# Performance work log

Hardware: AMD Instinct MI355X
Metric: run time of the kernel (lower is better)

The kernel has to match this reference:

```python
import jax, jax.numpy as jnp
import numpy as np

S = 2   # upsample scale
K = 5   # reassembly kernel k_up


def setup_inputs() -> dict:
    key = jax.random.key(0)
    ks = jax.random.split(key, 7)
    B, C, H, W = 4, 128, 64, 64
    C_MID = 64
    return {
        "x": jax.random.normal(ks[0], (B, C, H, W), dtype=jnp.float32),
        "w1": jax.random.normal(ks[1], (C_MID, C), dtype=jnp.float32) * 0.05,
        "w2": jax.random.normal(ks[2], (S * S * K * K, C_MID, 3, 3), dtype=jnp.float32) * 0.05,
        "bn_gamma": jax.random.uniform(ks[3], (C_MID,), dtype=jnp.float32, minval=0.5, maxval=1.5),
        "bn_beta": jax.random.normal(ks[4], (C_MID,), dtype=jnp.float32) * 0.1,
        "bn_mean": jax.random.normal(ks[5], (C_MID,), dtype=jnp.float32) * 0.1,
        "bn_var": jax.random.uniform(ks[6], (C_MID,), dtype=jnp.float32, minval=0.5, maxval=1.5),
    }


def reference(x, w1, w2, bn_gamma, bn_beta, bn_mean, bn_var):
    B, C, H, W = x.shape
    s, k = S, K
    eps = 1e-5
    # --- content encoder: 1x1 conv -> BN (inference form) -> ReLU -> 3x3 conv ---
    h = jnp.einsum('bchw,oc->bohw', x, w1)  # (B, c_mid, H, W)
    inv = bn_gamma / jnp.sqrt(bn_var + eps)
    h = h * inv[None, :, None, None] + (bn_beta - bn_mean * inv)[None, :, None, None]
    h = jax.nn.relu(h)
    ker = jax.lax.conv_general_dilated(
        h, w2, window_strides=(1, 1), padding=((1, 1), (1, 1)),
        dimension_numbers=('NCHW', 'OIHW', 'NCHW'))  # (B, s*s*k*k, H, W)
    # softmax over the k*k reassembly window
    ker = jax.nn.softmax(ker.reshape(B, s * s, k * k, H, W), axis=2)
    # --- unfold k x k neighborhoods of x (row-major window order, as F.unfold) ---
    p = k // 2
    xp = jnp.pad(x, ((0, 0), (0, 0), (p, p), (p, p)))
    patches = jnp.stack(
        [xp[:, :, i:i + H, j:j + W] for i in range(k) for j in range(k)],
        axis=2)  # (B, C, k*k, H, W)
    # weighted reassembly: sum over the k*k window per (sub-pixel, channel)
    out = jnp.einsum('bckhw,bskhw->bcshw', patches, ker)  # (B, C, s*s, H, W)
    # pixel shuffle: (B, C, s, s, H, W) -> (B, C, H*s, W*s)
    out = out.reshape(B, C, s, s, H, W).transpose(0, 1, 4, 2, 5, 3)
    return out.reshape(B, C, H * s, W * s)
```

## Files before the change

kernel.cpp:

```cpp
#include <hip/hip_runtime.h>
#include <hip/hip_bf16.h>

#define HW 4096

typedef __attribute__((ext_vector_type(8))) short  short8;
typedef __attribute__((ext_vector_type(4))) float  floatx4;

#define OFF_W2B 0ul
#define OFF_W1B 129024ul
#define OFF_BN  145408ul

__global__ __launch_bounds__(256) void prep_kernel(const float* __restrict__ w1,
                                                   const float* __restrict__ w2,
                                                   const float* __restrict__ gamma,
                                                   const float* __restrict__ beta,
                                                   const float* __restrict__ mean,
                                                   const float* __restrict__ var,
                                                   char* __restrict__ ws) {
    int tid = blockIdx.x * 256 + threadIdx.x;
    if (tid < 64512) {
        int n = tid / 576;
        int k = tid - n * 576;
        int t = k >> 6, c = k & 63;
        float v = (n < 100) ? w2[(n * 64 + c) * 9 + t] : 0.f;
        ((__hip_bfloat16*)(ws + OFF_W2B))[tid] = __float2bfloat16(v);
    } else if (tid < 64512 + 8192) {
        int i = tid - 64512;
        ((__hip_bfloat16*)(ws + OFF_W1B))[i] = __float2bfloat16(w1[i]);
    } else if (tid < 64512 + 8192 + 64) {
        int o = tid - 64512 - 8192;
        float inv = gamma[o] * rsqrtf(var[o] + 1e-5f);
        ((float2*)(ws + OFF_BN))[o] = make_float2(inv, beta[o] - mean[o] * inv);
    }
}

__global__ __launch_bounds__(1024, 1) void fused_carafe(const float* __restrict__ x,
                                                        const char* __restrict__ ws,
                                                        float* __restrict__ out) {
    __shared__ float xs[128 * 144];
    __shared__ __align__(16) __hip_bfloat16 hs[100 * 88];
    __shared__ __align__(16) char un[54784];
    __hip_bfloat16* xbh = (__hip_bfloat16*)un;
    float* lg = (float*)un;
    float* ks = (float*)(un + 29184);

    int b    = blockIdx.x >> 6;
    int tile = blockIdx.x & 63;
    int ty0 = (tile >> 3) << 3;
    int tx0 = (tile & 7) << 3;
    int tid = threadIdx.x;
    int lane = tid & 63, wave = tid >> 6;
    int q = lane >> 4, m = lane & 15;

    int nh  = wave & 1;
    int nt0 = nh * 2;
    const __hip_bfloat16* w1b = (const __hip_bfloat16*)(ws + OFF_W1B);
    short8 bw[2][4];
    #pragma unroll
    for (int j = 0; j < 2; ++j)
        #pragma unroll
        for (int s = 0; s < 4; ++s)
            bw[j][s] = *(const short8*)(w1b + ((nt0 + j) * 16 + m) * 128 + s * 32 + q * 8);

    const float* xb = x + (size_t)b * 128 * HW;
    #pragma unroll
    for (int i = 0; i < 18; ++i) {
        int idx = tid + i * 1024;
        int c = idx / 144, p = idx - c * 144;
        int hy = p / 12, hx = p - hy * 12;
        int gy = ty0 + hy - 2, gx = tx0 + hx - 2;
        float v = 0.f;
        if ((unsigned)gy < 64u && (unsigned)gx < 64u)
            v = xb[(size_t)c * HW + gy * 64 + gx];
        xs[idx] = v;
        if ((unsigned)(hy - 1) < 10u && (unsigned)(hx - 1) < 10u) {
            int hp = (hy - 1) * 10 + (hx - 1);
            xbh[hp * 136 + c] = __float2bfloat16(v);
        }
    }
    if (tid < 816) ((unsigned*)(xbh + 100 * 136))[tid] = 0u;
    __syncthreads();

    if (wave < 14) {
        int mt = wave >> 1;
        int pix = mt * 16 + m;
        floatx4 acc0, acc1;
        #pragma unroll
        for (int r = 0; r < 4; ++r) { acc0[r] = 0.f; acc1[r] = 0.f; }
        #pragma unroll
        for (int s = 0; s < 4; ++s) {
            short8 a = *(const short8*)(&xbh[pix * 136 + s * 32 + q * 8]);
            acc0 = __builtin_amdgcn_mfma_f32_16x16x32_bf16(a, bw[0][s], acc0, 0, 0, 0);
            acc1 = __builtin_amdgcn_mfma_f32_16x16x32_bf16(a, bw[1][s], acc1, 0, 0, 0);
        }
        const float2* bn = (const float2*)(ws + OFF_BN);
        int o0 = nt0 * 16 + m, o1 = (nt0 + 1) * 16 + m;
        float2 ia0 = bn[o0], ia1 = bn[o1];
        #pragma unroll
        for (int r = 0; r < 4; ++r) {
            int prow = mt * 16 + q * 4 + r;
            if (prow < 100) {
                int hy = prow / 10, hx = prow - hy * 10;
                int gy = ty0 + hy - 1, gx = tx0 + hx - 1;
                bool in = ((unsigned)gy < 64u) && ((unsigned)gx < 64u);
                float v0 = in ? fmaxf(fmaf(acc0[r], ia0.x, ia0.y), 0.f) : 0.f;
                float v1 = in ? fmaxf(fmaf(acc1[r], ia1.x, ia1.y), 0.f) : 0.f;
                hs[prow * 88 + o0] = __float2bfloat16(v0);
                hs[prow * 88 + o1] = __float2bfloat16(v1);
            }
        }
    }
    __syncthreads();

    {
        int mt = wave & 3, ng = wave >> 2;
        int pixidx = mt * 16 + m;
        int py = pixidx >> 3, px = pixidx & 7;
        int cn0 = ng * 2;
        int NT = (ng < 3) ? 2 : 1;

        const __hip_bfloat16* w2b = (const __hip_bfloat16*)(ws + OFF_W2B);
        const __hip_bfloat16* bp0 = w2b + (size_t)(cn0 * 16 + m) * 576 + q * 8;
        const __hip_bfloat16* bp1 = w2b + (size_t)((cn0 + 1) * 16 + m) * 576 + q * 8;

        floatx4 acc0, acc1;
        #pragma unroll
        for (int r = 0; r < 4; ++r) { acc0[r] = 0.f; acc1[r] = 0.f; }

        short8 b0 = *(const short8*)bp0;
        short8 b1 = (NT == 2) ? *(const short8*)bp1 : b0;

        for (int s = 0; s < 18; ++s) {
            int t = s >> 1, c0 = (s & 1) * 32;
            short8 a = *(const short8*)(&hs[((py + t / 3) * 10 + (px + t % 3)) * 88 + c0 + q * 8]);
            short8 n0 = b0, n1 = b1;
            if (s < 17) {
                int ko = (s + 1) * 32;
                n0 = *(const short8*)(bp0 + ko);
                if (NT == 2) n1 = *(const short8*)(bp1 + ko);
            }
            acc0 = __builtin_amdgcn_mfma_f32_16x16x32_bf16(a, b0, acc0, 0, 0, 0);
            if (NT == 2)
                acc1 = __builtin_amdgcn_mfma_f32_16x16x32_bf16(a, b1, acc1, 0, 0, 0);
            b0 = n0; b1 = n1;
        }
        #pragma unroll
        for (int r = 0; r < 4; ++r)
            lg[(mt * 16 + q * 4 + r) * 114 + cn0 * 16 + m] = acc0[r];
        if (NT == 2) {
            #pragma unroll
            for (int r = 0; r < 4; ++r)
                lg[(mt * 16 + q * 4 + r) * 114 + (cn0 + 1) * 16 + m] = acc1[r];
        }
    }
    __syncthreads();

    if (tid < 256) {
        int pix = tid & 63, g = tid >> 6;
        float v[25];
        #pragma unroll
        for (int wi = 0; wi < 25; ++wi) v[wi] = lg[pix * 114 + g * 25 + wi];
        float mx = v[0];
        #pragma unroll
        for (int wi = 1; wi < 25; ++wi) mx = fmaxf(mx, v[wi]);
        float ssum = 0.f;
        #pragma unroll
        for (int wi = 0; wi < 25; ++wi) { v[wi] = __expf(v[wi] - mx); ssum += v[wi]; }
        float rs = 1.f / ssum;
        #pragma unroll
        for (int t25 = 0; t25 < 25; ++t25)
            ks[(t25 * 4 + g) * 64 + pix] = v[t25] * rs;
    }
    __syncthreads();

    {
        int ch0 = wave * 8;
        int py = lane >> 3, px = lane & 7;
        int Y = ty0 + py, X = tx0 + px;

        float acc[32];
        #pragma unroll
        for (int i = 0; i < 32; ++i) acc[i] = 0.f;

        const float* xw = xs + ch0 * 144 + py * 12 + px;
        #pragma unroll 5
        for (int t = 0; t < 25; ++t) {
            int ti = t / 5, tj = t % 5;
            int po = ti * 12 + tj;
            float k0 = ks[(t * 4 + 0) * 64 + lane];
            float k1 = ks[(t * 4 + 1) * 64 + lane];
            float k2 = ks[(t * 4 + 2) * 64 + lane];
            float k3 = ks[(t * 4 + 3) * 64 + lane];
            #pragma unroll
            for (int i = 0; i < 8; ++i) {
                float xv = xw[i * 144 + po];
                acc[i * 4 + 0] = fmaf(xv, k0, acc[i * 4 + 0]);
                acc[i * 4 + 1] = fmaf(xv, k1, acc[i * 4 + 1]);
                acc[i * 4 + 2] = fmaf(xv, k2, acc[i * 4 + 2]);
                acc[i * 4 + 3] = fmaf(xv, k3, acc[i * 4 + 3]);
            }
        }

        #pragma unroll
        for (int i = 0; i < 8; ++i) {
            size_t o0 = (((size_t)b * 128 + ch0 + i) * 128 + 2 * Y) * 128 + 2 * X;
            *(float2*)(out + o0)       = make_float2(acc[i * 4 + 0], acc[i * 4 + 1]);
            *(float2*)(out + o0 + 128) = make_float2(acc[i * 4 + 2], acc[i * 4 + 3]);
        }
    }
}

extern "C" void kernel_launch(void* const* d_in, const int* in_sizes, int n_in,
                              void* d_out, int out_size, void* d_ws, size_t ws_size,
                              hipStream_t stream) {
    const float* x     = (const float*)d_in[0];
    const float* w1    = (const float*)d_in[1];
    const float* w2    = (const float*)d_in[2];
    const float* gamma = (const float*)d_in[3];
    const float* beta  = (const float*)d_in[4];
    const float* mean  = (const float*)d_in[5];
    const float* var   = (const float*)d_in[6];
    float* out = (float*)d_out;
    char*  ws  = (char*)d_ws;

    prep_kernel<<<285, 256, 0, stream>>>(w1, w2, gamma, beta, mean, var, ws);
    fused_carafe<<<256, 1024, 0, stream>>>(x, ws, out);
}
```

Baseline: 114.2 us.

## Halve spatial tile to 4x8, store x tile as bf16, double grid

The spatial tile shrinks from 8x8 to 4x8 pixels, so the grid grows to 512 blocks and the lower shared-memory footprint may let more blocks share a CU. The x halo tile is now kept only once, in bf16 channel-minor layout, and feeds both the 1x1-conv MFMA and the reassembly. The reassembly loop uses vectorized bf16 and float4 loads with a rearranged softmax-weight layout. The cost is that the reassembly now reads bf16 x instead of fp32, which lowers accuracy, and the smaller tile recomputes more halo work per block.

```diff
diff --git a/kernel.cpp b/kernel.cpp
--- a/kernel.cpp
+++ b/kernel.cpp
@@ -9,6 +9,10 @@
 #define OFF_W2B 0ul
 #define OFF_W1B 129024ul
 #define OFF_BN  145408ul
+
+__device__ __forceinline__ float bfbits(unsigned u) {
+    union { unsigned u; float f; } t; t.u = u; return t.f;
+}
 
 __global__ __launch_bounds__(256) void prep_kernel(const float* __restrict__ w1,
                                                    const float* __restrict__ w2,
@@ -34,129 +38,103 @@
     }
 }
 
-__global__ __launch_bounds__(1024, 1) void fused_carafe(const float* __restrict__ x,
+__global__ __launch_bounds__(1024, 8) void fused_carafe(const float* __restrict__ x,
                                                         const char* __restrict__ ws,
                                                         float* __restrict__ out) {
-    __shared__ float xs[128 * 144];
-    __shared__ __align__(16) __hip_bfloat16 hs[100 * 88];
-    __shared__ __align__(16) char un[54784];
-    __hip_bfloat16* xbh = (__hip_bfloat16*)un;
-    float* lg = (float*)un;
-    float* ks = (float*)(un + 29184);
-
-    int b    = blockIdx.x >> 6;
-    int tile = blockIdx.x & 63;
-    int ty0 = (tile >> 3) << 3;
-    int tx0 = (tile & 7) << 3;
+    __shared__ __align__(16) __hip_bfloat16 xs[96 * 136];
+    __shared__ __align__(16) __hip_bfloat16 hs[60 * 72];
+    __shared__ __align__(16) float lg[32 * 114];
+    __shared__ __align__(16) float ks[32 * 104];
+
+    int b    = blockIdx.x >> 7;
+    int tile = blockIdx.x & 127;
+    int ty0 = (tile >> 3) * 4;
+    int tx0 = (tile & 7) * 8;
     int tid = threadIdx.x;
     int lane = tid & 63, wave = tid >> 6;
     int q = lane >> 4, m = lane & 15;
 
-    int nh  = wave & 1;
-    int nt0 = nh * 2;
+    int bnt = wave >> 2;
+    int bo  = bnt * 16 + m;
     const __hip_bfloat16* w1b = (const __hip_bfloat16*)(ws + OFF_W1B);
-    short8 bw[2][4];
+    short8 bw[4];
     #pragma unroll
-    for (int j = 0; j < 2; ++j)
-        #pragma unroll
-        for (int s = 0; s < 4; ++s)
-            bw[j][s] = *(const short8*)(w1b + ((nt0 + j) * 16 + m) * 128 + s * 32 + q * 8);
+    for (int s = 0; s < 4; ++s)
+        bw[s] = *(const short8*)(w1b + bo * 128 + s * 32 + q * 8);
+    float2 bnia = ((const float2*)(ws + OFF_BN))[bo];
 
     const float* xb = x + (size_t)b * 128 * HW;
     #pragma unroll
-    for (int i = 0; i < 18; ++i) {
+    for (int i = 0; i < 12; ++i) {
         int idx = tid + i * 1024;
-        int c = idx / 144, p = idx - c * 144;
+        int c = idx / 96, p = idx - c * 96;
         int hy = p / 12, hx = p - hy * 12;
         int gy = ty0 + hy - 2, gx = tx0 + hx - 2;
         float v = 0.f;
         if ((unsigned)gy < 64u && (unsigned)gx < 64u)
             v = xb[(size_t)c * HW + gy * 64 + gx];
-        xs[idx] = v;
-        if ((unsigned)(hy - 1) < 10u && (unsigned)(hx - 1) < 10u) {
-            int hp = (hy - 1) * 10 + (hx - 1);
-            xbh[hp * 136 + c] = __float2bfloat16(v);
-        }
-    }
-    if (tid < 816) ((unsigned*)(xbh + 100 * 136))[tid] = 0u;
-    __syncthreads();
-
-    if (wave < 14) {
-        int mt = wave >> 1;
-        int pix = mt * 16 + m;
-        floatx4 acc0, acc1;
-        #pragma unroll
-        for (int r = 0; r < 4; ++r) { acc0[r] = 0.f; acc1[r] = 0.f; }
+        xs[p * 136 + c] = __float2bfloat16(v);
+    }
+    __syncthreads();
+
+    {
+        int mt = wave & 3;
+        int hp = mt * 16 + m;
+        int hy1 = hp / 10, hx1 = hp - hy1 * 10;
+        int xrow = (hy1 + 1) * 12 + (hx1 + 1);
+        floatx4 acc;
+        #pragma unroll
+        for (int r = 0; r < 4; ++r) acc[r] = 0.f;
         #pragma unroll
         for (int s = 0; s < 4; ++s) {
-            short8 a = *(const short8*)(&xbh[pix * 136 + s * 32 + q * 8]);
-            acc0 = __builtin_amdgcn_mfma_f32_16x16x32_bf16(a, bw[0][s], acc0, 0, 0, 0);
-            acc1 = __builtin_amdgcn_mfma_f32_16x16x32_bf16(a, bw[1][s], acc1, 0, 0, 0);
-        }
-        const float2* bn = (const float2*)(ws + OFF_BN);
-        int o0 = nt0 * 16 + m, o1 = (nt0 + 1) * 16 + m;
-        float2 ia0 = bn[o0], ia1 = bn[o1];
+            short8 a = *(const short8*)(&xs[xrow * 136 + s * 32 + q * 8]);
+            acc = __builtin_amdgcn_mfma_f32_16x16x32_bf16(a, bw[s], acc, 0, 0, 0);
+        }
         #pragma unroll
         for (int r = 0; r < 4; ++r) {
             int prow = mt * 16 + q * 4 + r;
-            if (prow < 100) {
-                int hy = prow / 10, hx = prow - hy * 10;
-                int gy = ty0 + hy - 1, gx = tx0 + hx - 1;
+            if (prow < 60) {
+                int phy = prow / 10, phx = prow - phy * 10;
+                int gy = ty0 + phy - 1, gx = tx0 + phx - 1;
                 bool in = ((unsigned)gy < 64u) && ((unsigned)gx < 64u);
-                float v0 = in ? fmaxf(fmaf(acc0[r], ia0.x, ia0.y), 0.f) : 0.f;
-                float v1 = in ? fmaxf(fmaf(acc1[r], ia1.x, ia1.y), 0.f) : 0.f;
-                hs[prow * 88 + o0] = __float2bfloat16(v0);
-                hs[prow * 88 + o1] = __float2bfloat16(v1);
+                float v = in ? fmaxf(fmaf(acc[r], bnia.x, bnia.y), 0.f) : 0.f;
+                hs[prow * 72 + bo] = __float2bfloat16(v);
             }
         }
     }
     __syncthreads();
 
     {
-        int mt = wave & 3, ng = wave >> 2;
-        int pixidx = mt * 16 + m;
-        int py = pixidx >> 3, px = pixidx & 7;
-        int cn0 = ng * 2;
-        int NT = (ng < 3) ? 2 : 1;
-
-        const __hip_bfloat16* w2b = (const __hip_bfloat16*)(ws + OFF_W2B);
-        const __hip_bfloat16* bp0 = w2b + (size_t)(cn0 * 16 + m) * 576 + q * 8;
-        const __hip_bfloat16* bp1 = w2b + (size_t)((cn0 + 1) * 16 + m) * 576 + q * 8;
-
-        floatx4 acc0, acc1;
-        #pragma unroll
-        for (int r = 0; r < 4; ++r) { acc0[r] = 0.f; acc1[r] = 0.f; }
-
-        short8 b0 = *(const short8*)bp0;
-        short8 b1 = (NT == 2) ? *(const short8*)bp1 : b0;
-
-        for (int s = 0; s < 18; ++s) {
-            int t = s >> 1, c0 = (s & 1) * 32;
-            short8 a = *(const short8*)(&hs[((py + t / 3) * 10 + (px + t % 3)) * 88 + c0 + q * 8]);
-            short8 n0 = b0, n1 = b1;
-            if (s < 17) {
-                int ko = (s + 1) * 32;
-                n0 = *(const short8*)(bp0 + ko);
-                if (NT == 2) n1 = *(const short8*)(bp1 + ko);
+        int mt = wave & 1, nt = wave >> 1;
+        if (nt < 7) {
+            int pixidx = mt * 16 + m;
+            int py = pixidx >> 3, px = pixidx & 7;
+            const __hip_bfloat16* w2b = (const __hip_bfloat16*)(ws + OFF_W2B);
+            const __hip_bfloat16* bp  = w2b + (size_t)(nt * 16 + m) * 576 + q * 8;
+
+            floatx4 acc;
+            #pragma unroll
+            for (int r = 0; r < 4; ++r) acc[r] = 0.f;
+
+            short8 bcur = *(const short8*)bp;
+            for (int s = 0; s < 18; ++s) {
+                int t = s >> 1, c0 = (s & 1) * 32;
+                int ti = t / 3, tj = t - ti * 3;
+                short8 a = *(const short8*)(&hs[((py + ti) * 10 + px + tj) * 72 + c0 + q * 8]);
+                short8 bn2 = bcur;
+                if (s < 17) bn2 = *(const short8*)(bp + (s + 1) * 32);
+                acc = __builtin_amdgcn_mfma_f32_16x16x32_bf16(a, bcur, acc, 0, 0, 0);
+                bcur = bn2;
             }
-            acc0 = __builtin_amdgcn_mfma_f32_16x16x32_bf16(a, b0, acc0, 0, 0, 0);
-            if (NT == 2)
-                acc1 = __builtin_amdgcn_mfma_f32_16x16x32_bf16(a, b1, acc1, 0, 0, 0);
-            b0 = n0; b1 = n1;
-        }
-        #pragma unroll
-        for (int r = 0; r < 4; ++r)
-            lg[(mt * 16 + q * 4 + r) * 114 + cn0 * 16 + m] = acc0[r];
-        if (NT == 2) {
             #pragma unroll
             for (int r = 0; r < 4; ++r)
-                lg[(mt * 16 + q * 4 + r) * 114 + (cn0 + 1) * 16 + m] = acc1[r];
-        }
-    }
-    __syncthreads();
-
-    if (tid < 256) {
-        int pix = tid & 63, g = tid >> 6;
+                lg[(mt * 16 + q * 4 + r) * 114 + nt * 16 + m] = acc[r];
+        }
+    }
+    __syncthreads();
+
+    if (tid < 128) {
+        int pix = tid & 31, g = tid >> 5;
         float v[25];
         #pragma unroll
         for (int wi = 0; wi < 25; ++wi) v[wi] = lg[pix * 114 + g * 25 + wi];
@@ -169,41 +147,44 @@
         float rs = 1.f / ssum;
         #pragma unroll
         for (int t25 = 0; t25 < 25; ++t25)
-            ks[(t25 * 4 + g) * 64 + pix] = v[t25] * rs;
+            ks[pix * 104 + t25 * 4 + g] = v[t25] * rs;
     }
     __syncthreads();
 
     {
-        int ch0 = wave * 8;
-        int py = lane >> 3, px = lane & 7;
+        int pix   = lane & 31;
+        int chsub = lane >> 5;
+        int chb   = wave * 8 + chsub * 4;
+        int py = pix >> 3, px = pix & 7;
         int Y = ty0 + py, X = tx0 + px;
 
-        float acc[32];
-        #pragma unroll
-        for (int i = 0; i < 32; ++i) acc[i] = 0.f;
-
-        const float* xw = xs + ch0 * 144 + py * 12 + px;
+        float acc[16];
+        #pragma unroll
+        for (int i = 0; i < 16; ++i) acc[i] = 0.f;
+
         #pragma unroll 5
         for (int t = 0; t < 25; ++t) {
-            int ti = t / 5, tj = t % 5;
-            int po = ti * 12 + tj;
-            float k0 = ks[(t * 4 + 0) * 64 + lane];
-            float k1 = ks[(t * 4 + 1) * 64 + lane];
-            float k2 = ks[(t * 4 + 2) * 64 + lane];
-            float k3 = ks[(t * 4 + 3) * 64 + lane];
+            int ti = t / 5, tj = t - ti * 5;
+            int xrow = (py + ti) * 12 + (px + tj);
+            uint2 xv = *(const uint2*)(&xs[xrow * 136 + chb]);
+            float4 kv = *(const float4*)(&ks[pix * 104 + t * 4]);
+            float xf[4];
+            xf[0] = bfbits(xv.x << 16);
+            xf[1] = bfbits(xv.x & 0xFFFF0000u);
+            xf[2] = bfbits(xv.y << 16);
+            xf[3] = bfbits(xv.y & 0xFFFF0000u);
             #pragma unroll
-            for (int i = 0; i < 8; ++i) {
-                float xv = xw[i * 144 + po];
-                acc[i * 4 + 0] = fmaf(xv, k0, acc[i * 4 + 0]);
-                acc[i * 4 + 1] = fmaf(xv, k1, acc[i * 4 + 1]);
-                acc[i * 4 + 2] = fmaf(xv, k2, acc[i * 4 + 2]);
-                acc[i * 4 + 3] = fmaf(xv, k3, acc[i * 4 + 3]);
+            for (int i = 0; i < 4; ++i) {
+                acc[i * 4 + 0] = fmaf(xf[i], kv.x, acc[i * 4 + 0]);
+                acc[i * 4 + 1] = fmaf(xf[i], kv.y, acc[i * 4 + 1]);
+                acc[i * 4 + 2] = fmaf(xf[i], kv.z, acc[i * 4 + 2]);
+                acc[i * 4 + 3] = fmaf(xf[i], kv.w, acc[i * 4 + 3]);
             }
         }
 
         #pragma unroll
-        for (int i = 0; i < 8; ++i) {
-            size_t o0 = (((size_t)b * 128 + ch0 + i) * 128 + 2 * Y) * 128 + 2 * X;
+        for (int i = 0; i < 4; ++i) {
+            size_t o0 = (((size_t)b * 128 + chb + i) * 128 + 2 * Y) * 128 + 2 * X;
             *(float2*)(out + o0)       = make_float2(acc[i * 4 + 0], acc[i * 4 + 1]);
             *(float2*)(out + o0 + 128) = make_float2(acc[i * 4 + 2], acc[i * 4 + 3]);
         }
@@ -224,5 +205,5 @@
     char*  ws  = (char*)d_ws;
 
     prep_kernel<<<285, 256, 0, stream>>>(w1, w2, gamma, beta, mean, var, ws);
-    fused_carafe<<<256, 1024, 0, stream>>>(x, ws, out);
-}
+    fused_carafe<<<512, 1024, 0, stream>>>(x, ws, out);
+}
```

Result: faster. 108.8 us (-4.7%).
